# Performance work log

Hardware: AMD Instinct MI355X
Metric: run time of the kernel (lower is better)

The kernel has to match this reference:

```python
import jax, jax.numpy as jnp
import numpy as np

B, T, N = 256, 50, 32          # graphs per batch, timesteps, nodes per scene graph
FIN, HG, HR, HFC = 16, 64, 64, 128  # gnn in, gnn hidden, gnn out (== HG, shared LayerNorm), gru hidden
DS, DTG, OST, OCA = 32, 32, 8, 8    # sensor dim, target dim, stimuli classes, cause classes


def _ln(x, g, b, eps=1e-5):
    m = jnp.mean(x, axis=-1, keepdims=True)
    v = jnp.var(x, axis=-1, keepdims=True)
    return (x - m) * jax.lax.rsqrt(v + eps) * g + b


def _gru_seq(x, Wi, Wh, bi, bh):
    # x: [B, T, Din] -> [B, T, H]; PyTorch GRU gate order (r, z, n)
    xp = x @ Wi + bi  # precompute input projections for all timesteps
    H = Wh.shape[0]
    h0 = jnp.zeros((x.shape[0], H), x.dtype)
    def step(h, xt):
        gh = h @ Wh + bh
        ir, iz, ig = jnp.split(xt, 3, axis=-1)
        hr, hz, hg = jnp.split(gh, 3, axis=-1)
        r = jax.nn.sigmoid(ir + hr)
        z = jax.nn.sigmoid(iz + hz)
        n = jnp.tanh(ig + r * hg)
        hn = (1.0 - z) * n + z * h
        return hn, hn
    _, ys = jax.lax.scan(step, h0, jnp.swapaxes(xp, 0, 1))
    return jnp.swapaxes(ys, 0, 1)


def _glorot(key, shape):
    s = jnp.sqrt(2.0 / (shape[0] + shape[-1]))
    return jax.random.normal(key, shape, jnp.float32) * s


def setup_inputs() -> dict:
    key = jax.random.key(0)
    ks = jax.random.split(key, 24)
    inp = {
        'feat': jax.random.normal(ks[0], (B, T, N, FIN), jnp.float32),
        'sensor': jax.random.normal(ks[1], (B, T, DS), jnp.float32),
        'target': jax.random.normal(ks[2], (B, T, DTG), jnp.float32),
        'adj': jax.random.randint(ks[3], (B, T, N, N), 0, 2, jnp.int32),
        'W_g1': _glorot(ks[4], (FIN, HG)), 'b_g1': jnp.zeros((HG,)),
        'W_g3': _glorot(ks[5], (HG, HR)), 'b_g3': jnp.zeros((HR,)),
        'ln_g_g': jnp.ones((HG,)), 'ln_g_b': jnp.zeros((HG,)),
    }
    for i, (sfx, din) in enumerate([('G', HR), ('S', DS), ('T', DTG)]):
        inp['Wi' + sfx] = _glorot(ks[6 + 2 * i], (din, 3 * HFC))
        inp['Wh' + sfx] = _glorot(ks[7 + 2 * i], (HFC, 3 * HFC))
        inp['bi' + sfx] = jnp.zeros((3 * HFC,))
        inp['bh' + sfx] = jnp.zeros((3 * HFC,))
    inp['W_fc1'] = _glorot(ks[12], (3 * HFC, HFC)); inp['b_fc1'] = jnp.zeros((HFC,))
    inp['ln_fc_g'] = jnp.ones((HFC,)); inp['ln_fc_b'] = jnp.zeros((HFC,))
    inp['W_st'] = _glorot(ks[13], (HFC, OST)); inp['b_st'] = jnp.zeros((OST,))
    inp['W_ca'] = _glorot(ks[14], (HFC, OCA)); inp['b_ca'] = jnp.zeros((OCA,))
    return inp


def reference(feat, sensor, target, W_g1, b_g1, W_g3, b_g3, ln_g_g, ln_g_b,
              WiG, WhG, biG, bhG, WiS, WhS, biS, bhS, WiT, WhT, biT, bhT,
              W_fc1, b_fc1, ln_fc_g, ln_fc_b, W_st, b_st, W_ca, b_ca, adj):
    # Batched mean-aggregation GNN (self-loops avoid zero in-degree), fused over all B*T graphs.
    adj_f = adj.astype(jnp.float32) + jnp.eye(N, dtype=jnp.float32)
    deg = jnp.sum(adj_f, axis=-1, keepdims=True)  # [B,T,N,1]
    def gnn(h, W, b):
        agg = jnp.einsum('btij,btjf->btif', adj_f, h) / deg
        return jax.nn.relu(_ln(agg @ W + b, ln_g_g, ln_g_b))  # linear -> norm -> relu (dropout=0)
    h1 = gnn(feat, W_g1, b_g1)   # gnn1c
    h2 = gnn(h1, W_g3, b_g3)     # gnn3c
    graph_seq = h2[:, :, 0, :]   # hG[0]: node-0 readout per (graph, timestep) -> [B,T,HR]
    gG = _gru_seq(graph_seq, WiG, WhG, biG, bhG)
    gS = _gru_seq(sensor, WiS, WhS, biS, bhS)
    gT = _gru_seq(target, WiT, WhT, biT, bhT)
    out = jnp.concatenate([gG, gS, gT], axis=-1).reshape(-1, 3 * HFC)  # [B*T, 384]
    h = jax.nn.relu(_ln(out @ W_fc1 + b_fc1, ln_fc_g, ln_fc_b))
    return (h @ W_st + b_st, h @ W_ca + b_ca)
```

## Files before the change

### kernel.cpp

```cpp
#include <hip/hip_runtime.h>
#include <stdint.h>

typedef unsigned short u16;

#define DI __device__ __forceinline__

DI float b2f(u16 u){ union{ unsigned int i; float f; } v; v.i = ((unsigned int)u)<<16; return v.f; }
DI u16 f2bf(float f){ union{ float f; unsigned int u; } v; v.f = f;
  unsigned int u = v.u; return (u16)((u + 0x7FFFu + ((u>>16)&1u)) >> 16); }
DI float ubf_lo(unsigned w){ union{ unsigned u; float f; } v; v.u = w<<16; return v.f; }
DI float ubf_hi(unsigned w){ union{ unsigned u; float f; } v; v.u = w & 0xFFFF0000u; return v.f; }
DI float sigm_(float x){ return 1.0f/(1.0f + __expf(-x)); }
DI float tanh_(float x){ x = fminf(fmaxf(x,-15.0f),15.0f); float e = __expf(2.0f*x); return (e-1.0f)/(e+1.0f); }

DI bool probe_bf(const void* ones){ return ((const u16*)ones)[0] == 0x3F80u; }

template<bool BF>
DI float ld(const void* p, long i){
  if constexpr (BF) return b2f(((const u16*)p)[i]);
  else              return ((const float*)p)[i];
}

typedef _Float16 f16x2 __attribute__((ext_vector_type(2)));
DI unsigned pk2(float lo, float hi){
  union{ f16x2 h; unsigned u; } v;
  v.h[0] = (_Float16)lo; v.h[1] = (_Float16)hi;
  return v.u;
}
DI float dot2(unsigned w, unsigned x, float c){
  union{ unsigned u; f16x2 h; } a, b;
  a.u = w; b.u = x;
  return __builtin_amdgcn_fdot2(a.h, b.h, c, false);
}
DI u16 cvt1(float v){ union{ _Float16 h; u16 u; } c; c.h = (_Float16)v; return c.u; }
DI float h2f(u16 u){ union{ u16 u2; _Float16 h; } c; c.u2 = u; return (float)c.h; }
DI float h2f_lo(unsigned w){ return h2f((u16)(w & 0xFFFFu)); }
DI float h2f_hi(unsigned w){ return h2f((u16)(w >> 16)); }

constexpr int T_ = 50;
constexpr int BT = 256*50;

template<bool BF>
__global__ __launch_bounds__(256) void k_gnn(
    const int* __restrict__ adj, const void* __restrict__ feat,
    const void* __restrict__ Wg1, const void* __restrict__ bg1,
    const void* __restrict__ Wg3, const void* __restrict__ bg3,
    const void* __restrict__ lng, const void* __restrict__ lnb,
    u16* __restrict__ gs)
{
  if(probe_bf(lng) != BF) return;

  __shared__ __align__(16) unsigned s_adjh[32*20];
  __shared__ __align__(16) unsigned s_feath[16*20];
  __shared__ float s_dinv[32];
  __shared__ float s_b1[64], s_b3[64], s_lg[64], s_lb[64];
  __shared__ __align__(16) u16 s_ag1h[32*24];
  __shared__ __align__(16) u16 s_z1h[32*72];
  __shared__ float s_m[32], s_r[32];
  __shared__ __align__(16) float s_p2[256];
  __shared__ __align__(16) float s_q2[256];

  const int tid = threadIdx.x;
  const long bt = blockIdx.x;
  const unsigned ONE2 = 0x3C003C00u;

  unsigned w1ch[8];
  float wg3r[16];
  {
    int o = tid&63, fg = tid>>6;
    #pragma unroll
    for(int p=0;p<8;p++)
      w1ch[p] = pk2(ld<BF>(Wg1,(2*p)*64+o), ld<BF>(Wg1,(2*p+1)*64+o));
    #pragma unroll
    for(int ff=0;ff<16;ff++)
      wg3r[ff] = ld<BF>(Wg3,(fg*16+ff)*64+o);
  }

  {
    const int4* ap4 = (const int4*)(adj + bt*1024);
    int4 v = ap4[tid];
    int i = tid>>3, j0 = (tid&7)*4;
    float f0 = (float)v.x + (i==j0   ? 1.0f : 0.0f);
    float f1 = (float)v.y + (i==j0+1 ? 1.0f : 0.0f);
    float f2 = (float)v.z + (i==j0+2 ? 1.0f : 0.0f);
    float f3 = (float)v.w + (i==j0+3 ? 1.0f : 0.0f);
    uint2 pw; pw.x = pk2(f0,f1); pw.y = pk2(f2,f3);
    *(uint2*)&s_adjh[i*20 + (tid&7)*2] = pw;

    int f = tid&15, rp = tid>>4;
    float lo = ld<BF>(feat, bt*512 + (long)(2*rp  )*16 + f);
    float hi = ld<BF>(feat, bt*512 + (long)(2*rp+1)*16 + f);
    s_feath[f*20 + rp] = pk2(lo,hi);

    if(tid<64){ s_b1[tid]=ld<BF>(bg1,tid); s_b3[tid]=ld<BF>(bg3,tid);
                s_lg[tid]=ld<BF>(lng,tid); s_lb[tid]=ld<BF>(lnb,tid); }
  }
  __syncthreads();

  #pragma unroll
  for(int rep=0; rep<2; rep++){
    int idx = tid + rep*256;
    int i = idx>>4, f = idx&15;
    const uint4* A4 = (const uint4*)&s_adjh[i*20];
    const uint4* F4 = (const uint4*)&s_feath[f*20];
    uint4 a0=A4[0], a1=A4[1], a2=A4[2], a3=A4[3];
    uint4 b0=F4[0], b1v=F4[1], b2=F4[2], b3v=F4[3];
    float c0 = dot2(a0.x,b0.x, dot2(a0.y,b0.y, dot2(a0.z,b0.z, dot2(a0.w,b0.w, 0.f))));
    float c1 = dot2(a1.x,b1v.x, dot2(a1.y,b1v.y, dot2(a1.z,b1v.z, dot2(a1.w,b1v.w, 0.f))));
    float c2 = dot2(a2.x,b2.x, dot2(a2.y,b2.y, dot2(a2.z,b2.z, dot2(a2.w,b2.w, 0.f))));
    float c3 = dot2(a3.x,b3v.x, dot2(a3.y,b3v.y, dot2(a3.z,b3v.z, dot2(a3.w,b3v.w, 0.f))));
    s_ag1h[i*24+f] = cvt1((c0+c1)+(c2+c3));
  }
  if(tid<32){
    const uint4* A4 = (const uint4*)&s_adjh[tid*20];
    uint4 a0=A4[0], a1=A4[1], a2=A4[2], a3=A4[3];
    float c0 = dot2(a0.x,ONE2, dot2(a0.y,ONE2, dot2(a0.z,ONE2, dot2(a0.w,ONE2, 0.f))));
    float c1 = dot2(a1.x,ONE2, dot2(a1.y,ONE2, dot2(a1.z,ONE2, dot2(a1.w,ONE2, 0.f))));
    float c2 = dot2(a2.x,ONE2, dot2(a2.y,ONE2, dot2(a2.z,ONE2, dot2(a2.w,ONE2, 0.f))));
    float c3 = dot2(a3.x,ONE2, dot2(a3.y,ONE2, dot2(a3.z,ONE2, dot2(a3.w,ONE2, 0.f))));
    s_dinv[tid] = 1.0f/((c0+c1)+(c2+c3));
  }
  __syncthreads();

  #pragma unroll
  for(int rep=0; rep<8; rep++){
    int idx = tid + rep*256;
    int i = idx>>6, o = idx&63;
    const uint4* G = (const uint4*)&s_ag1h[i*24];
    uint4 g0 = G[0], g1 = G[1];
    float c0 = dot2(w1ch[0],g0.x, dot2(w1ch[1],g0.y, 0.f));
    float c1 = dot2(w1ch[2],g0.z, dot2(w1ch[3],g0.w, 0.f));
    float c2 = dot2(w1ch[4],g1.x, dot2(w1ch[5],g1.y, 0.f));
    float c3 = dot2(w1ch[6],g1.z, dot2(w1ch[7],g1.w, 0.f));
    float z = ((c0+c1)+(c2+c3))*s_dinv[i] + s_b1[o];
    s_z1h[i*72+o] = cvt1(z);
  }
  __syncthreads();

  if(tid<32){
    const uint4* Z = (const uint4*)&s_z1h[tid*72];
    float s0=0.f,s1=0.f,q0=0.f,q1=0.f;
    #pragma unroll
    for(int k=0;k<8;k+=2){
      uint4 z0 = Z[k], z1v = Z[k+1];
      s0 = dot2(z0.x,ONE2, dot2(z0.y,ONE2, dot2(z0.z,ONE2, dot2(z0.w,ONE2, s0))));
      q0 = dot2(z0.x,z0.x, dot2(z0.y,z0.y, dot2(z0.z,z0.z, dot2(z0.w,z0.w, q0))));
      s1 = dot2(z1v.x,ONE2, dot2(z1v.y,ONE2, dot2(z1v.z,ONE2, dot2(z1v.w,ONE2, s1))));
      q1 = dot2(z1v.x,z1v.x, dot2(z1v.y,z1v.y, dot2(z1v.z,z1v.z, dot2(z1v.w,z1v.w, q1))));
    }
    float s = s0+s1, q = q0+q1;
    float m = s*(1.0f/64.0f);
    float var = q*(1.0f/64.0f) - m*m;
    s_m[tid]=m; s_r[tid]=rsqrtf(var + 1e-5f);
  }
  __syncthreads();

  {
    int o = tid&63, jg = tid>>6;
    float lg_o = s_lg[o], lb_o = s_lb[o];
    const float4* M4 = (const float4*)&s_m[jg*8];
    const float4* R4 = (const float4*)&s_r[jg*8];
    float4 m0=M4[0], m1=M4[1], r0=R4[0], r1=R4[1];
    float mj[8] = {m0.x,m0.y,m0.z,m0.w,m1.x,m1.y,m1.z,m1.w};
    float rj[8] = {r0.x,r0.y,r0.z,r0.w,r1.x,r1.y,r1.z,r1.w};
    uint4 ap = *(const uint4*)&s_adjh[jg*4];
    float aw[8] = {h2f_lo(ap.x),h2f_hi(ap.x),h2f_lo(ap.y),h2f_hi(ap.y),
                   h2f_lo(ap.z),h2f_hi(ap.z),h2f_lo(ap.w),h2f_hi(ap.w)};
    float s=0.f;
    #pragma unroll
    for(int jj=0;jj<8;jj++){
      float zv = h2f(s_z1h[(jg*8+jj)*72 + o]);
      float h = fmaxf((zv - mj[jj])*rj[jj]*lg_o + lb_o, 0.0f);
      s += aw[jj]*h;
    }
    s_p2[jg*64+o] = s;
  }
  __syncthreads();

  {
    int o = tid&63, fg = tid>>6;
    float dinv0 = s_dinv[0];
    const float4* P0 = (const float4*)&s_p2[       fg*16];
    const float4* P1 = (const float4*)&s_p2[ 64 +  fg*16];
    const float4* P2 = (const float4*)&s_p2[128 +  fg*16];
    const float4* P3 = (const float4*)&s_p2[192 +  fg*16];
    float acc=0.f;
    #pragma unroll
    for(int q=0;q<4;q++){
      float4 x0=P0[q], x1=P1[q], x2=P2[q], x3=P3[q];
      float a2x = (x0.x+x1.x+x2.x+x3.x)*dinv0;
      float a2y = (x0.y+x1.y+x2.y+x3.y)*dinv0;
      float a2z = (x0.z+x1.z+x2.z+x3.z)*dinv0;
      float a2w = (x0.w+x1.w+x2.w+x3.w)*dinv0;
      acc += a2x*wg3r[4*q] + a2y*wg3r[4*q+1] + a2z*wg3r[4*q+2] + a2w*wg3r[4*q+3];
    }
    s_q2[fg*64+o] = acc;
  }
  __syncthreads();

  if(tid<64){
    float z = s_q2[tid]+s_q2[64+tid]+s_q2[128+tid]+s_q2[192+tid] + s_b3[tid];
    s_p2[tid] = z;
    s_q2[tid] = z*z;
    #pragma unroll
    for(int off=32; off>=1; off>>=1){
      if(tid<off){ s_p2[tid]+=s_p2[tid+off]; s_q2[tid]+=s_q2[tid+off]; }
    }
    float m = s_p2[0]*(1.0f/64.0f);
    float var = s_q2[0]*(1.0f/64.0f) - m*m;
    float r = rsqrtf(var+1e-5f);
    float v = (z-m)*r*s_lg[tid] + s_lb[tid];
    gs[bt*64+tid] = f2bf(fmaxf(v,0.0f));
  }
}

template<bool BF>
__global__ __launch_bounds__(384) void k_xp(
    const u16* __restrict__ gs,
    const void* __restrict__ sen, const void* __restrict__ tgt,
    const void* __restrict__ WiG, const void* __restrict__ biG,
    const void* __restrict__ WiS, const void* __restrict__ biS,
    const void* __restrict__ WiT, const void* __restrict__ biT,
    const void* __restrict__ probe, u16* __restrict__ xp)
{
  if(probe_bf(probe) != BF) return;

  __shared__ unsigned s_wi[32*384];
  __shared__ __align__(16) unsigned s_xr[32*32];

  const int tid = threadIdx.x;
  const int g = blockIdx.y;
  const long R0 = (long)blockIdx.x*32;
  const void* Wi = (g==0)?WiG:((g==1)?WiS:WiT);
  const void* bi = (g==0)?biG:((g==1)?biS:biT);
  const int kp = (g==0)?32:16;

  for(int k2=0;k2<kp;k2++)
    s_wi[k2*384+tid] = pk2(ld<BF>(Wi,(long)(2*k2  )*384+tid),
                           ld<BF>(Wi,(long)(2*k2+1)*384+tid));
  if(g==0){
    const unsigned* x32 = (const unsigned*)gs;
    for(int idx=tid; idx<1024; idx+=384){
      int r = idx>>5, k2 = idx&31;
      unsigned w = x32[(R0+r)*32 + k2];
      s_xr[r*32+k2] = pk2(ubf_lo(w), ubf_hi(w));
    }
  } else {
    const void* src = (g==1)?sen:tgt;
    for(int idx=tid; idx<512; idx+=384){
      int r = idx>>4, k2 = idx&15;
      long base = (R0+r)*32 + 2*k2;
      s_xr[r*16+k2] = pk2(ld<BF>(src,base), ld<BF>(src,base+1));
    }
  }
  __syncthreads();

  const int c = tid;
  const float bi_c = ld<BF>(bi,c);
  float acc[32];
  #pragma unroll
  for(int r=0;r<32;r++) acc[r]=0.f;

  const uint4* xr4 = (const uint4*)s_xr;
  if(g==0){
    #pragma unroll
    for(int q=0;q<8;q++){
      unsigned w0=s_wi[(4*q+0)*384+c], w1=s_wi[(4*q+1)*384+c];
      unsigned w2=s_wi[(4*q+2)*384+c], w3=s_wi[(4*q+3)*384+c];
      #pragma unroll
      for(int r=0;r<32;r++){
        uint4 xv = xr4[r*8+q];
        acc[r] = dot2(w0,xv.x, dot2(w1,xv.y, dot2(w2,xv.z, dot2(w3,xv.w, acc[r]))));
      }
    }
  } else {
    #pragma unroll
    for(int q=0;q<4;q++){
      unsigned w0=s_wi[(4*q+0)*384+c], w1=s_wi[(4*q+1)*384+c];
      unsigned w2=s_wi[(4*q+2)*384+c], w3=s_wi[(4*q+3)*384+c];
      #pragma unroll
      for(int r=0;r<32;r++){
        uint4 xv = xr4[r*4+q];
        acc[r] = dot2(w0,xv.x, dot2(w1,xv.y, dot2(w2,xv.z, dot2(w3,xv.w, acc[r]))));
      }
    }
  }

  u16* xpo = xp + ((long)g*BT + R0)*384;
  #pragma unroll
  for(int r=0;r<32;r++)
    xpo[(long)r*384 + c] = cvt1(acc[r] + bi_c);
}

typedef _Float16 f16x8 __attribute__((ext_vector_type(8)));
typedef float f32x4 __attribute__((ext_vector_type(4)));

template<bool BF>
__global__ __launch_bounds__(512, 1) void k_rec(
    const u16* __restrict__ xp,
    const void* __restrict__ WhG, const void* __restrict__ bhG,
    const void* __restrict__ WhS, const void* __restrict__ bhS,
    const void* __restrict__ WhT, const void* __restrict__ bhT,
    const void* __restrict__ probe, u16* __restrict__ gout)
{
  if(probe_bf(probe) != BF) return;

  __shared__ __align__(16) _Float16 s_whf[6144*8];
  __shared__ __align__(16) _Float16 s_h[2][16*136];

  const int tid = threadIdx.x;
  const int g = blockIdx.y;
  const int row0 = blockIdx.x*16;
  const void* Wh = (g==0)?WhG:((g==1)?WhS:WhT);
  const void* bh = (g==0)?bhG:((g==1)?bhS:bhT);

  for(int idx=tid; idx<6144; idx+=512){
    int lane = idx&63, fr = idx>>6;
    int w = fr/12, rem = fr - w*12, gg = rem>>2, kk = rem&3;
    int c  = gg*128 + w*16 + (lane&15);
    int kb = kk*32 + ((lane>>4)<<3);
    f16x8 v;
    #pragma unroll
    for(int jj=0;jj<8;jj++) v[jj] = (_Float16)ld<BF>(Wh, (long)(kb+jj)*384 + c);
    *(f16x8*)&s_whf[idx*8] = v;
  }
  for(int idx=tid; idx<2*16*136; idx+=512) ((_Float16*)s_h)[idx] = (_Float16)0.f;
  __syncthreads();

  const int l = tid&63, w = tid>>6;
  const int c  = w*16 + (l&15);
  const int rb = (l>>4)*4;
  const int arow  = l&15;
  const int akoff = (l>>4)<<3;
  const int fb = w*12;

  const float bh0 = ld<BF>(bh, c);
  const float bh1 = ld<BF>(bh, 128+c);
  const float bh2 = ld<BF>(bh, 256+c);

  float h_own[4] = {0.f,0.f,0.f,0.f};

  const long xpB = ((long)g*BT + (long)row0*T_)*384;
  const u16* xp0 = xp + xpB + (long)(rb+0)*T_*384 + c;
  const u16* xp1 = xp + xpB + (long)(rb+1)*T_*384 + c;
  const u16* xp2 = xp + xpB + (long)(rb+2)*T_*384 + c;
  const u16* xp3 = xp + xpB + (long)(rb+3)*T_*384 + c;
  u16* go0 = gout + (long)g*BT*128 + (long)(row0+rb+0)*T_*128 + c;
  u16* go1 = go0 + (long)T_*128;
  u16* go2 = go1 + (long)T_*128;
  u16* go3 = go2 + (long)T_*128;

  u16 xq[12];
  xq[0]=xp0[0];   xq[1]=xp1[0];   xq[2]=xp2[0];   xq[3]=xp3[0];
  xq[4]=xp0[128]; xq[5]=xp1[128]; xq[6]=xp2[128]; xq[7]=xp3[128];
  xq[8]=xp0[256]; xq[9]=xp1[256]; xq[10]=xp2[256]; xq[11]=xp3[256];

  int cur = 0;
  for(int t=0;t<T_;t++){
    u16 xqn[12];
    if(t+1<T_){
      xqn[0]=xp0[384]; xqn[1]=xp1[384]; xqn[2]=xp2[384]; xqn[3]=xp3[384];
      xqn[4]=xp0[512]; xqn[5]=xp1[512]; xqn[6]=xp2[512]; xqn[7]=xp3[512];
      xqn[8]=xp0[640]; xqn[9]=xp1[640]; xqn[10]=xp2[640]; xqn[11]=xp3[640];
    }

    f32x4 ar={0.f,0.f,0.f,0.f}, az={0.f,0.f,0.f,0.f}, an={0.f,0.f,0.f,0.f};
    #pragma unroll
    for(int kk=0;kk<4;kk++){
      f16x8 av = *(const f16x8*)&s_h[cur][arow*136 + kk*32 + akoff];
      f16x8 br = *(const f16x8*)&s_whf[((fb + 0 + kk)*64 + l)*8];
      f16x8 bz = *(const f16x8*)&s_whf[((fb + 4 + kk)*64 + l)*8];
      f16x8 bn = *(const f16x8*)&s_whf[((fb + 8 + kk)*64 + l)*8];
      ar = __builtin_amdgcn_mfma_f32_16x16x32_f16(av, br, ar, 0, 0, 0);
      az = __builtin_amdgcn_mfma_f32_16x16x32_f16(av, bz, az, 0, 0, 0);
      an = __builtin_amdgcn_mfma_f32_16x16x32_f16(av, bn, an, 0, 0, 0);
    }

    _Float16* hw = &s_h[cur^1][0];
    {
      float r0g = sigm_(h2f(xq[0]) + ar[0] + bh0);
      float z0g = sigm_(h2f(xq[4]) + az[0] + bh1);
      float n0g = tanh_(h2f(xq[8]) + r0g*(an[0] + bh2));
      float h0 = (1.0f-z0g)*n0g + z0g*h_own[0];
      h_own[0] = h0; hw[(rb+0)*136 + c] = (_Float16)h0; go0[0] = f2bf(h0);

      float r1g = sigm_(h2f(xq[1]) + ar[1] + bh0);
      float z1g = sigm_(h2f(xq[5]) + az[1] + bh1);
      float n1g = tanh_(h2f(xq[9]) + r1g*(an[1] + bh2));
      float h1 = (1.0f-z1g)*n1g + z1g*h_own[1];
      h_own[1] = h1; hw[(rb+1)*136 + c] = (_Float16)h1; go1[0] = f2bf(h1);

      float r2g = sigm_(h2f(xq[2]) + ar[2] + bh0);
      float z2g = sigm_(h2f(xq[6]) + az[2] + bh1);
      float n2g = tanh_(h2f(xq[10]) + r2g*(an[2] + bh2));
      float h2 = (1.0f-z2g)*n2g + z2g*h_own[2];
      h_own[2] = h2; hw[(rb+2)*136 + c] = (_Float16)h2; go2[0] = f2bf(h2);

      float r3g = sigm_(h2f(xq[3]) + ar[3] + bh0);
      float z3g = sigm_(h2f(xq[7]) + az[3] + bh1);
      float n3g = tanh_(h2f(xq[11]) + r3g*(an[3] + bh2));
      float h3 = (1.0f-z3g)*n3g + z3g*h_own[3];
      h_own[3] = h3; hw[(rb+3)*136 + c] = (_Float16)h3; go3[0] = f2bf(h3);
    }

    asm volatile("s_waitcnt lgkmcnt(0)" ::: "memory");
    __builtin_amdgcn_s_barrier();
    cur ^= 1;
    #pragma unroll
    for(int q=0;q<12;q++) xq[q] = xqn[q];
    xp0 += 384; xp1 += 384; xp2 += 384; xp3 += 384;
    go0 += 128; go1 += 128; go2 += 128; go3 += 128;
  }
}

template<bool BF>
__global__ __launch_bounds__(384, 3) void k_gru_f(
    const u16* __restrict__ gs,
    const void* __restrict__ sen, const void* __restrict__ tgt,
    const void* __restrict__ WiG, const void* __restrict__ biG,
    const void* __restrict__ WiS, const void* __restrict__ biS,
    const void* __restrict__ WiT, const void* __restrict__ biT,
    const void* __restrict__ WhG, const void* __restrict__ bhG,
    const void* __restrict__ WhS, const void* __restrict__ bhS,
    const void* __restrict__ WhT, const void* __restrict__ bhT,
    const void* __restrict__ probe, u16* __restrict__ gout)
{
  if(probe_bf(probe) != BF) return;

  __shared__ __align__(16) uint4 s_wh4[16*384];
  __shared__ __align__(4) u16 s_xp[T_*384];
  __shared__ __align__(16) unsigned s_x[T_*32];
  __shared__ __align__(16) u16 s_hu[128];
  __shared__ float s_r[128], s_z[128];

  const int tid = threadIdx.x;
  const int g = blockIdx.y;
  const long row = blockIdx.x;
  const void* Wi = (g==0)?WiG:((g==1)?WiS:WiT);
  const void* bi = (g==0)?biG:((g==1)?biS:biT);
  const void* Wh = (g==0)?WhG:((g==1)?WhS:WhT);
  const void* bh = (g==0)?bhG:((g==1)?bhS:bhT);
  const int din = (g==0)?64:32;
  const int kmax = din>>1;

  #pragma unroll
  for(int p=0;p<16;p++){
    uint4 v;
    v.x = pk2(ld<BF>(Wh,(long)(8*p+0)*384+tid), ld<BF>(Wh,(long)(8*p+1)*384+tid));
    v.y = pk2(ld<BF>(Wh,(long)(8*p+2)*384+tid), ld<BF>(Wh,(long)(8*p+3)*384+tid));
    v.z = pk2(ld<BF>(Wh,(long)(8*p+4)*384+tid), ld<BF>(Wh,(long)(8*p+5)*384+tid));
    v.w = pk2(ld<BF>(Wh,(long)(8*p+6)*384+tid), ld<BF>(Wh,(long)(8*p+7)*384+tid));
    s_wh4[p*384+tid] = v;
  }

  unsigned wi2[32];
  #pragma unroll
  for(int k2=0;k2<32;k2++){
    if(k2<kmax){
      float lo = ld<BF>(Wi,(long)(2*k2  )*384+tid);
      float hi = ld<BF>(Wi,(long)(2*k2+1)*384+tid);
      wi2[k2] = pk2(lo,hi);
    } else wi2[k2] = 0u;
  }

  const float bi_t = ld<BF>(bi,tid);
  const float bh_t = ld<BF>(bh,tid);

  if(g==0){
    const unsigned* xr = (const unsigned*)(gs + row*(T_*64));
    for(int idx=tid; idx<T_*32; idx+=384){
      unsigned w = xr[idx];
      s_x[idx] = pk2(ubf_lo(w), ubf_hi(w));
    }
  } else {
    const void* src = (g==1)?sen:tgt;
    const long base0 = (long)row*(T_*32);
    for(int idx=tid; idx<T_*16; idx+=384){
      float lo = ld<BF>(src, base0 + 2*idx);
      float hi = ld<BF>(src, base0 + 2*idx+1);
      s_x[idx] = pk2(lo,hi);
    }
  }
  if(tid<64) ((unsigned*)s_hu)[tid] = 0u;
  __syncthreads();

  if(g==0){
    const uint4* x4 = (const uint4*)s_x;
    for(int t=0;t<T_;t++){
      float a0=0.f,a1=0.f,a2=0.f,a3=0.f;
      #pragma unroll
      for(int q=0;q<8;q++){
        uint4 xv = x4[t*8+q];
        a0 = dot2(wi2[4*q+0], xv.x, a0);
        a1 = dot2(wi2[4*q+1], xv.y, a1);
        a2 = dot2(wi2[4*q+2], xv.z, a2);
        a3 = dot2(wi2[4*q+3], xv.w, a3);
      }
      s_xp[t*384+tid] = f2bf(((a0+a1)+(a2+a3)) + bi_t);
    }
  } else {
    const uint4* x4 = (const uint4*)s_x;
    for(int t=0;t<T_;t++){
      float a0=0.f,a1=0.f,a2=0.f,a3=0.f;
      #pragma unroll
      for(int q=0;q<4;q++){
        uint4 xv = x4[t*4+q];
        a0 = dot2(wi2[4*q+0], xv.x, a0);
        a1 = dot2(wi2[4*q+1], xv.y, a1);
        a2 = dot2(wi2[4*q+2], xv.z, a2);
        a3 = dot2(wi2[4*q+3], xv.w, a3);
      }
      s_xp[t*384+tid] = f2bf(((a0+a1)+(a2+a3)) + bi_t);
    }
  }
  __syncthreads();

  const int seg = tid>>7, j = tid&127;
  float h_own = 0.f;

  for(int t=0;t<T_;t++){
    const uint4* h4 = (const uint4*)s_hu;
    float a0=0.f,a1=0.f,a2=0.f,a3=0.f;
    #pragma unroll
    for(int p=0;p<16;p++){
      uint4 wv = s_wh4[p*384+tid];
      uint4 hv = h4[p];
      a0 = dot2(wv.x, hv.x, a0);
      a1 = dot2(wv.y, hv.y, a1);
      a2 = dot2(wv.z, hv.z, a2);
      a3 = dot2(wv.w, hv.w, a3);
    }
    float gh = ((a0+a1)+(a2+a3)) + bh_t;
    float xp_own = b2f(s_xp[t*384+tid]);
    if(seg==0)      s_r[j] = sigm_(xp_own + gh);
    else if(seg==1) s_z[j] = sigm_(xp_own + gh);
    __syncthreads();
    if(seg==2){
      float r = s_r[j], z = s_z[j];
      float n = tanh_(xp_own + r*gh);
      float hn = (1.0f-z)*n + z*h_own;
      h_own = hn;
      s_hu[j] = cvt1(hn);
      s_xp[t*384+j] = f2bf(hn);
    }
    __syncthreads();
  }

  u16* go = gout + ((long)g*BT + row*T_)*128;
  const unsigned* sx32 = (const unsigned*)s_xp;
  unsigned* go32 = (unsigned*)go;
  for(int idx2=tid; idx2<3200; idx2+=384){
    int e0 = idx2*2;
    int t = e0>>7, jj = e0&127;
    go32[(t*128+jj)>>1] = sx32[(t*384+jj)>>1];
  }
}

template<bool BF>
__global__ __launch_bounds__(256) void k_head(
    const u16* __restrict__ gout,
    const void* __restrict__ Wfc, const void* __restrict__ bfc,
    const void* __restrict__ lg, const void* __restrict__ lb,
    const void* __restrict__ Wst, const void* __restrict__ bst,
    const void* __restrict__ Wca, const void* __restrict__ bca,
    void* __restrict__ out)
{
  if(probe_bf(lg) != BF) return;

  __shared__ __align__(16) float s_oT[384*8];
  __shared__ __align__(16) float s_z[8*132];
  __shared__ __align__(16) float s_h[8*132];
  __shared__ float s_mr[16];
  const int tid=threadIdx.x;
  const long r0 = (long)blockIdx.x*8;

  for(int idx=tid; idx<8*384; idx+=256){
    int r = idx/384, c = idx - r*384;
    int seg = c>>7, j = c&127;
    s_oT[c*8+r] = b2f(gout[(long)seg*BT*128 + (r0+r)*128 + j]);
  }
  __syncthreads();

  const int o = tid&127, rs = tid>>7;
  float acc[4]={0,0,0,0};
  for(int k=0;k<384;k++){
    float wv = ld<BF>(Wfc, (long)k*128+o);
    float4 hv = *(const float4*)&s_oT[k*8 + rs*4];
    acc[0] += hv.x*wv; acc[1] += hv.y*wv; acc[2] += hv.z*wv; acc[3] += hv.w*wv;
  }
  float bv = ld<BF>(bfc,o);
  #pragma unroll
  for(int rr=0;rr<4;rr++) s_z[(rs*4+rr)*132 + o] = acc[rr] + bv;
  __syncthreads();

  if(tid<8){
    const float4* zr = (const float4*)(s_z + tid*132);
    float4 s4={0.f,0.f,0.f,0.f}, q4={0.f,0.f,0.f,0.f};
    #pragma unroll
    for(int k=0;k<32;k++){
      float4 v = zr[k];
      s4.x+=v.x; s4.y+=v.y; s4.z+=v.z; s4.w+=v.w;
      q4.x+=v.x*v.x; q4.y+=v.y*v.y; q4.z+=v.z*v.z; q4.w+=v.w*v.w;
    }
    float s = (s4.x+s4.y)+(s4.z+s4.w);
    float qq = (q4.x+q4.y)+(q4.z+q4.w);
    float m=s*(1.0f/128.0f), var=qq*(1.0f/128.0f)-m*m;
    s_mr[tid]=m; s_mr[8+tid]=rsqrtf(var+1e-5f);
  }
  __syncthreads();

  #pragma unroll
  for(int rep=0; rep<4; rep++){
    int idx = tid + rep*256;
    int r = idx>>7, j = idx&127;
    float v = (s_z[r*132+j]-s_mr[r])*s_mr[8+r]*ld<BF>(lg,j) + ld<BF>(lb,j);
    s_h[r*132+j]=fmaxf(v,0.f);
  }
  __syncthreads();

  if(tid<128){
    int r = tid>>4, oo = tid&15;
    int which = oo>>3, oc = oo&7;
    const void* W = which? Wca : Wst;
    const void* bb = which? bca : bst;
    float s=0.f;
    for(int k=0;k<128;k++) s += s_h[r*132+k]*ld<BF>(W,(long)k*8+oc);
    s += ld<BF>(bb,oc);
    long pos = (long)which*BT*8 + (r0+r)*8 + oc;
    if constexpr (BF) ((u16*)out)[pos]  = f2bf(s);
    else              ((float*)out)[pos] = s;
  }
}

extern "C" void kernel_launch(void* const* d_in, const int* in_sizes, int n_in,
                              void* d_out, int out_size, void* d_ws, size_t ws_size,
                              hipStream_t stream)
{
  const void* feat  = d_in[0];
  const void* sen   = d_in[1];
  const void* tgt   = d_in[2];
  const int*  adj   = (const int*)d_in[3];
  const void* Wg1   = d_in[4];
  const void* bg1   = d_in[5];
  const void* Wg3   = d_in[6];
  const void* bg3   = d_in[7];
  const void* lng   = d_in[8];
  const void* lnb   = d_in[9];
  const void* WiG   = d_in[10];
  const void* WhG   = d_in[11];
  const void* biG   = d_in[12];
  const void* bhG   = d_in[13];
  const void* WiS   = d_in[14];
  const void* WhS   = d_in[15];
  const void* biS   = d_in[16];
  const void* bhS   = d_in[17];
  const void* WiT   = d_in[18];
  const void* WhT   = d_in[19];
  const void* biT   = d_in[20];
  const void* bhT   = d_in[21];
  const void* Wfc   = d_in[22];
  const void* bfc   = d_in[23];
  const void* lfg   = d_in[24];
  const void* lfb   = d_in[25];
  const void* Wst   = d_in[26];
  const void* bst   = d_in[27];
  const void* Wca   = d_in[28];
  const void* bca   = d_in[29];

  u16* gs = (u16*)d_ws;
  u16* go = gs + (long)BT*64;
  u16* xw = go + (long)3*BT*128;
  const size_t NEED = ((size_t)BT*64 + (size_t)3*BT*128 + (size_t)3*BT*384)*2;

  k_gnn<true ><<<dim3(BT), dim3(256), 0, stream>>>(adj, feat, Wg1, bg1, Wg3, bg3, lng, lnb, gs);
  k_gnn<false><<<dim3(BT), dim3(256), 0, stream>>>(adj, feat, Wg1, bg1, Wg3, bg3, lng, lnb, gs);

  if(ws_size >= NEED){
    k_xp<true ><<<dim3(400,3), dim3(384), 0, stream>>>(gs, sen, tgt,
        WiG, biG, WiS, biS, WiT, biT, lng, xw);
    k_xp<false><<<dim3(400,3), dim3(384), 0, stream>>>(gs, sen, tgt,
        WiG, biG, WiS, biS, WiT, biT, lng, xw);
    k_rec<true ><<<dim3(16,3), dim3(512), 0, stream>>>(xw,
        WhG, bhG, WhS, bhS, WhT, bhT, lng, go);
    k_rec<false><<<dim3(16,3), dim3(512), 0, stream>>>(xw,
        WhG, bhG, WhS, bhS, WhT, bhT, lng, go);
  } else {
    k_gru_f<true ><<<dim3(256,3), dim3(384), 0, stream>>>(gs, sen, tgt,
        WiG, biG, WiS, biS, WiT, biT, WhG, bhG, WhS, bhS, WhT, bhT, lng, go);
    k_gru_f<false><<<dim3(256,3), dim3(384), 0, stream>>>(gs, sen, tgt,
        WiG, biG, WiS, biS, WiT, biT, WhG, bhG, WhS, bhS, WhT, bhT, lng, go);
  }

  k_head<true ><<<dim3(BT/8), dim3(256), 0, stream>>>(go, Wfc, bfc, lfg, lfb, Wst, bst, Wca, bca, d_out);
  k_head<false><<<dim3(BT/8), dim3(256), 0, stream>>>(go, Wfc, bfc, lfg, lfb, Wst, bst, Wca, bca, d_out);
}
```

Before: 341.4 us.

## Pre-pack recurrent weight fragments and keep them in registers instead of LDS

Adds a small kernel that converts each GRU's Wh into MFMA B-fragment layout (fp16) in workspace once per call. The recurrent kernel then loads its 12 fragments straight into registers rather than building a 96KB LDS copy. This removes per-step LDS reads of weights and the slow strided conversion done in every block's prologue. In exchange it adds an extra kernel launch and more register pressure, and it relies on the workspace being large enough.

```diff
diff --git a/kernel.cpp b/kernel.cpp
--- a/kernel.cpp
+++ b/kernel.cpp
@@ -292,40 +292,48 @@
     xpo[(long)r*384 + c] = cvt1(acc[r] + bi_c);
 }
 
-typedef _Float16 f16x8 __attribute__((ext_vector_type(8)));
-typedef float f32x4 __attribute__((ext_vector_type(4)));
-
 template<bool BF>
-__global__ __launch_bounds__(512, 1) void k_rec(
-    const u16* __restrict__ xp,
-    const void* __restrict__ WhG, const void* __restrict__ bhG,
-    const void* __restrict__ WhS, const void* __restrict__ bhS,
-    const void* __restrict__ WhT, const void* __restrict__ bhT,
-    const void* __restrict__ probe, u16* __restrict__ gout)
+__global__ __launch_bounds__(512) void k_wfrag(
+    const void* __restrict__ WhG, const void* __restrict__ WhS,
+    const void* __restrict__ WhT, const void* __restrict__ probe,
+    u16* __restrict__ wf)
 {
   if(probe_bf(probe) != BF) return;
-
-  __shared__ __align__(16) _Float16 s_whf[6144*8];
-  __shared__ __align__(16) _Float16 s_h[2][16*136];
-
+  const int g = blockIdx.x;
+  const void* Wh = (g==0)?WhG:((g==1)?WhS:WhT);
+  u16* out = wf + (long)g*6144*8;
   const int tid = threadIdx.x;
-  const int g = blockIdx.y;
-  const int row0 = blockIdx.x*16;
-  const void* Wh = (g==0)?WhG:((g==1)?WhS:WhT);
-  const void* bh = (g==0)?bhG:((g==1)?bhS:bhT);
-
   for(int idx=tid; idx<6144; idx+=512){
     int lane = idx&63, fr = idx>>6;
     int w = fr/12, rem = fr - w*12, gg = rem>>2, kk = rem&3;
     int c  = gg*128 + w*16 + (lane&15);
     int kb = kk*32 + ((lane>>4)<<3);
-    f16x8 v;
-    #pragma unroll
-    for(int jj=0;jj<8;jj++) v[jj] = (_Float16)ld<BF>(Wh, (long)(kb+jj)*384 + c);
-    *(f16x8*)&s_whf[idx*8] = v;
-  }
+    #pragma unroll
+    for(int jj=0;jj<8;jj++)
+      out[(long)idx*8+jj] = cvt1(ld<BF>(Wh,(long)(kb+jj)*384+c));
+  }
+}
+
+typedef _Float16 f16x8 __attribute__((ext_vector_type(8)));
+typedef float f32x4 __attribute__((ext_vector_type(4)));
+
+template<bool BF>
+__global__ __launch_bounds__(512, 1) void k_rec(
+    const u16* __restrict__ xp, const u16* __restrict__ wf,
+    const void* __restrict__ bhG, const void* __restrict__ bhS,
+    const void* __restrict__ bhT,
+    const void* __restrict__ probe, u16* __restrict__ gout)
+{
+  if(probe_bf(probe) != BF) return;
+
+  __shared__ __align__(16) _Float16 s_h[2][16*136];
+
+  const int tid = threadIdx.x;
+  const int g = blockIdx.y;
+  const int row0 = blockIdx.x*16;
+  const void* bh = (g==0)?bhG:((g==1)?bhS:bhT);
+
   for(int idx=tid; idx<2*16*136; idx+=512) ((_Float16*)s_h)[idx] = (_Float16)0.f;
-  __syncthreads();
 
   const int l = tid&63, w = tid>>6;
   const int c  = w*16 + (l&15);
@@ -333,6 +341,14 @@
   const int arow  = l&15;
   const int akoff = (l>>4)<<3;
   const int fb = w*12;
+
+  const u16* wfg = wf + (long)g*6144*8;
+  const long fbase = ((long)fb*64 + l)*8;
+  #define LDF(i) (*(const f16x8*)&wfg[fbase + (i)*512])
+  f16x8 b00=LDF(0),  b01=LDF(1),  b02=LDF(2),  b03=LDF(3);
+  f16x8 b10=LDF(4),  b11=LDF(5),  b12=LDF(6),  b13=LDF(7);
+  f16x8 b20=LDF(8),  b21=LDF(9),  b22=LDF(10), b23=LDF(11);
+  #undef LDF
 
   const float bh0 = ld<BF>(bh, c);
   const float bh1 = ld<BF>(bh, 128+c);
@@ -355,6 +371,8 @@
   xq[4]=xp0[128]; xq[5]=xp1[128]; xq[6]=xp2[128]; xq[7]=xp3[128];
   xq[8]=xp0[256]; xq[9]=xp1[256]; xq[10]=xp2[256]; xq[11]=xp3[256];
 
+  __syncthreads();
+
   int cur = 0;
   for(int t=0;t<T_;t++){
     u16 xqn[12];
@@ -365,15 +383,23 @@
     }
 
     f32x4 ar={0.f,0.f,0.f,0.f}, az={0.f,0.f,0.f,0.f}, an={0.f,0.f,0.f,0.f};
-    #pragma unroll
-    for(int kk=0;kk<4;kk++){
-      f16x8 av = *(const f16x8*)&s_h[cur][arow*136 + kk*32 + akoff];
-      f16x8 br = *(const f16x8*)&s_whf[((fb + 0 + kk)*64 + l)*8];
-      f16x8 bz = *(const f16x8*)&s_whf[((fb + 4 + kk)*64 + l)*8];
-      f16x8 bn = *(const f16x8*)&s_whf[((fb + 8 + kk)*64 + l)*8];
-      ar = __builtin_amdgcn_mfma_f32_16x16x32_f16(av, br, ar, 0, 0, 0);
-      az = __builtin_amdgcn_mfma_f32_16x16x32_f16(av, bz, az, 0, 0, 0);
-      an = __builtin_amdgcn_mfma_f32_16x16x32_f16(av, bn, an, 0, 0, 0);
+    {
+      f16x8 a0v = *(const f16x8*)&s_h[cur][arow*136 +  0 + akoff];
+      ar = __builtin_amdgcn_mfma_f32_16x16x32_f16(a0v, b00, ar, 0, 0, 0);
+      az = __builtin_amdgcn_mfma_f32_16x16x32_f16(a0v, b10, az, 0, 0, 0);
+      an = __builtin_amdgcn_mfma_f32_16x16x32_f16(a0v, b20, an, 0, 0, 0);
+      f16x8 a1v = *(const f16x8*)&s_h[cur][arow*136 + 32 + akoff];
+      ar = __builtin_amdgcn_mfma_f32_16x16x32_f16(a1v, b01, ar, 0, 0, 0);
+      az = __builtin_amdgcn_mfma_f32_16x16x32_f16(a1v, b11, az, 0, 0, 0);
+      an = __builtin_amdgcn_mfma_f32_16x16x32_f16(a1v, b21, an, 0, 0, 0);
+      f16x8 a2v = *(const f16x8*)&s_h[cur][arow*136 + 64 + akoff];
+      ar = __builtin_amdgcn_mfma_f32_16x16x32_f16(a2v, b02, ar, 0, 0, 0);
+      az = __builtin_amdgcn_mfma_f32_16x16x32_f16(a2v, b12, az, 0, 0, 0);
+      an = __builtin_amdgcn_mfma_f32_16x16x32_f16(a2v, b22, an, 0, 0, 0);
+      f16x8 a3v = *(const f16x8*)&s_h[cur][arow*136 + 96 + akoff];
+      ar = __builtin_amdgcn_mfma_f32_16x16x32_f16(a3v, b03, ar, 0, 0, 0);
+      az = __builtin_amdgcn_mfma_f32_16x16x32_f16(a3v, b13, az, 0, 0, 0);
+      an = __builtin_amdgcn_mfma_f32_16x16x32_f16(a3v, b23, an, 0, 0, 0);
     }
 
     _Float16* hw = &s_h[cur^1][0];
@@ -670,20 +696,24 @@
   u16* gs = (u16*)d_ws;
   u16* go = gs + (long)BT*64;
   u16* xw = go + (long)3*BT*128;
-  const size_t NEED = ((size_t)BT*64 + (size_t)3*BT*128 + (size_t)3*BT*384)*2;
+  u16* wfp= xw + (long)3*BT*384;
+  const size_t NEED = ((size_t)BT*64 + (size_t)3*BT*128 + (size_t)3*BT*384
+                       + (size_t)3*6144*8)*2;
 
   k_gnn<true ><<<dim3(BT), dim3(256), 0, stream>>>(adj, feat, Wg1, bg1, Wg3, bg3, lng, lnb, gs);
   k_gnn<false><<<dim3(BT), dim3(256), 0, stream>>>(adj, feat, Wg1, bg1, Wg3, bg3, lng, lnb, gs);
 
   if(ws_size >= NEED){
+    k_wfrag<true ><<<dim3(3), dim3(512), 0, stream>>>(WhG, WhS, WhT, lng, wfp);
+    k_wfrag<false><<<dim3(3), dim3(512), 0, stream>>>(WhG, WhS, WhT, lng, wfp);
     k_xp<true ><<<dim3(400,3), dim3(384), 0, stream>>>(gs, sen, tgt,
         WiG, biG, WiS, biS, WiT, biT, lng, xw);
     k_xp<false><<<dim3(400,3), dim3(384), 0, stream>>>(gs, sen, tgt,
         WiG, biG, WiS, biS, WiT, biT, lng, xw);
-    k_rec<true ><<<dim3(16,3), dim3(512), 0, stream>>>(xw,
-        WhG, bhG, WhS, bhS, WhT, bhT, lng, go);
-    k_rec<false><<<dim3(16,3), dim3(512), 0, stream>>>(xw,
-        WhG, bhG, WhS, bhS, WhT, bhT, lng, go);
+    k_rec<true ><<<dim3(16,3), dim3(512), 0, stream>>>(xw, wfp,
+        bhG, bhS, bhT, lng, go);
+    k_rec<false><<<dim3(16,3), dim3(512), 0, stream>>>(xw, wfp,
+        bhG, bhS, bhT, lng, go);
   } else {
     k_gru_f<true ><<<dim3(256,3), dim3(384), 0, stream>>>(gs, sen, tgt,
         WiG, biG, WiS, biS, WiT, biT, WhG, bhG, WhS, bhS, WhT, bhT, lng, go);
```

Result: no change. 335.4 us (-1.8%).
